# Optimization experiments

Hardware: AMD Instinct MI355X
Metric: run time of the kernel (lower is better)

Reference implementation:

```python
import jax, jax.numpy as jnp
import numpy as np

DIM = 1024
HEADS = 8
DIM_HEAD = 64
INNER = HEADS * DIM_HEAD  # 512


def setup_inputs() -> dict:
    key = jax.random.key(0)
    k1, k2, k3, k4 = jax.random.split(key, 4)
    x = jax.random.normal(k1, (4, 4096, DIM), dtype=jnp.float32)
    # torch nn.Linear weights: [out_features, in_features]
    w_qkv = jax.random.normal(k2, (INNER * 3, DIM), dtype=jnp.float32) * (DIM ** -0.5)
    w_out = jax.random.normal(k3, (DIM, INNER), dtype=jnp.float32) * (INNER ** -0.5)
    b_out = jax.random.normal(k4, (DIM,), dtype=jnp.float32) * 0.01
    return {"x": x, "w_qkv": w_qkv, "w_out": w_out, "b_out": b_out}


def reference(x, w_qkv, w_out, b_out):
    b, n, _ = x.shape
    h, dh = HEADS, DIM_HEAD
    qkv = x @ w_qkv.T  # [b, n, 3*inner]
    q, k, v = jnp.split(qkv, 3, axis=-1)
    # [b, n, inner] -> [b, h, n, dh]
    reshape = lambda t: t.reshape(b, n, h, dh).transpose(0, 2, 1, 3)
    q, k, v = reshape(q), reshape(k), reshape(v)
    k = jax.nn.softmax(k, axis=-1)
    context = jnp.einsum('bhnd,bhne->bhde', k, v)   # [b, h, dh, dh]
    out = jnp.einsum('bhnd,bhde->bhne', q, context)  # [b, h, n, dh]
    out = out.transpose(0, 2, 1, 3).reshape(b, n, h * dh)
    return out @ w_out.T + b_out
```

## Files before the change

### kernel.cpp

```cpp
#include <hip/hip_runtime.h>
#include <hip/hip_bf16.h>

using bf16 = __hip_bfloat16;
typedef __attribute__((ext_vector_type(8))) short short8;
typedef __attribute__((ext_vector_type(4))) float floatx4;

#define NB 4
#define NSEQ 4096
#define DIM 1024
#define INNER 512
#define TOK (NB * NSEQ)


__device__ inline unsigned short f2bf(float x) {
  union { bf16 h; unsigned short u; } c; c.h = __float2bfloat16(x); return c.u;
}
__device__ inline float bf2f(unsigned short u) {
  return __uint_as_float((unsigned)u << 16);
}
__device__ inline uint4 pack8(const float4 a, const float4 b) {
  union { uint4 u; unsigned short h[8]; } p;
  p.h[0] = f2bf(a.x); p.h[1] = f2bf(a.y); p.h[2] = f2bf(a.z); p.h[3] = f2bf(a.w);
  p.h[4] = f2bf(b.x); p.h[5] = f2bf(b.y); p.h[6] = f2bf(b.z); p.h[7] = f2bf(b.w);
  return p.u;
}

__device__ inline void gload_lds16(const bf16* g, bf16* ldsbase) {
  __builtin_amdgcn_global_load_lds(
      (const __attribute__((address_space(1))) void*)g,
      (__attribute__((address_space(3))) void*)ldsbase, 16, 0, 0);
}

__global__ __launch_bounds__(256)
void conv_wkv(const float* __restrict__ w_qkv, bf16* __restrict__ wkvb) {
  const size_t i = (size_t)blockIdx.x * 256 + threadIdx.x;
  const float* src = w_qkv + (size_t)INNER * DIM + i * 8;
  const float4 a = ((const float4*)src)[0];
  const float4 b = ((const float4*)src)[1];
  *(uint4*)(wkvb + i * 8) = pack8(a, b);
}

__global__ __launch_bounds__(256, 4)
void kv_softmax_ctx(const float* __restrict__ x, const bf16* __restrict__ wkvb,
                    float* __restrict__ ctx_part) {
  __shared__ __align__(16) char smem[33280];
  bf16* As = (bf16*)smem;
  bf16* Bs = (bf16*)(smem + 16384);
  unsigned short* skT = (unsigned short*)smem;
  unsigned short* vT  = (unsigned short*)(smem + 16640);

  const int tid    = threadIdx.x;
  const int p      = blockIdx.x;
  const int h      = (p >> 3) & 7;
  const int m_tile = (p & 7) + (p >> 6) * 8;
  const int m0     = m_tile * 128;

  const int wave = tid >> 6;
  const int lane = tid & 63;
  const int wr   = (wave >> 1) * 64;
  const int wc   = (wave & 1) * 64;
  const int quad = lane >> 4;
  const int r16  = lane & 15;
  const int rxor = r16 & 7;
  const int lrow = lane >> 3;
  const int lcol = lane & 7;
  const int gchunk = lcol ^ lrow;
  const int wb   = wave * 8 + lrow;

  const float* Ax = x + (size_t)(m0 + wb) * 1024 + lcol * 8;

  floatx4 acc[4][4];
#pragma unroll
  for (int i = 0; i < 4; ++i)
#pragma unroll
    for (int j = 0; j < 4; ++j) acc[i][j] = (floatx4)0.0f;

  for (int kt = 0; kt < 16; ++kt) {
    const int k0 = kt << 6;
#pragma unroll
    for (int t = 0; t < 4; ++t) {
      const int s   = wave * 4 + t;
      const int row = s * 8 + lrow;
      const int badd = (s * 8 >= 64) ? (448 + h * 64) : (h * 64);
      gload_lds16(wkvb + (size_t)(badd + row) * 1024 + k0 + gchunk * 8, Bs + s * 512);
    }
    float4 rA[8];
#pragma unroll
    for (int l = 0; l < 4; ++l) {
      rA[2 * l]     = *(const float4*)(Ax + (size_t)l * 32768 + k0);
      rA[2 * l + 1] = *(const float4*)(Ax + (size_t)l * 32768 + k0 + 4);
    }
#pragma unroll
    for (int l = 0; l < 4; ++l) {
      const int row = l * 32 + wb;
      *(uint4*)(As + row * 64 + ((lcol ^ lrow) << 3)) = pack8(rA[2 * l], rA[2 * l + 1]);
    }
    __syncthreads();
#pragma unroll
    for (int kk = 0; kk < 64; kk += 32) {
      const int cbase = kk >> 3;
      short8 af[4], bfg[4];
#pragma unroll
      for (int i = 0; i < 4; ++i)
        af[i] = *(const short8*)(As + (wr + i * 16 + r16) * 64 + (((quad + cbase) ^ rxor) << 3));
#pragma unroll
      for (int j = 0; j < 4; ++j)
        bfg[j] = *(const short8*)(Bs + (wc + j * 16 + r16) * 64 + (((quad + cbase) ^ rxor) << 3));
#pragma unroll
      for (int i = 0; i < 4; ++i)
#pragma unroll
        for (int j = 0; j < 4; ++j)
          acc[i][j] = __builtin_amdgcn_mfma_f32_16x16x32_bf16(af[i], bfg[j], acc[i][j], 0, 0, 0);
    }
    __syncthreads();
  }

  const int rowbase = wr + quad * 4;
  if ((wave & 1) == 0) {
#pragma unroll
    for (int i = 0; i < 4; ++i)
#pragma unroll
      for (int reg = 0; reg < 4; ++reg) {
        float kf[4];
#pragma unroll
        for (int j = 0; j < 4; ++j) kf[j] = bf2f(f2bf(acc[i][j][reg]));
        float mx = fmaxf(fmaxf(kf[0], kf[1]), fmaxf(kf[2], kf[3]));
        mx = fmaxf(mx, __shfl_xor(mx, 1, 64));
        mx = fmaxf(mx, __shfl_xor(mx, 2, 64));
        mx = fmaxf(mx, __shfl_xor(mx, 4, 64));
        mx = fmaxf(mx, __shfl_xor(mx, 8, 64));
        float e[4]; float s = 0.0f;
#pragma unroll
        for (int j = 0; j < 4; ++j) { e[j] = __expf(kf[j] - mx); s += e[j]; }
        s += __shfl_xor(s, 1, 64);
        s += __shfl_xor(s, 2, 64);
        s += __shfl_xor(s, 4, 64);
        s += __shfl_xor(s, 8, 64);
        const float inv = 1.0f / s;
        const int row = rowbase + i * 16 + reg;
#pragma unroll
        for (int j = 0; j < 4; ++j)
          skT[(j * 16 + r16) * 130 + row] = f2bf(e[j] * inv);
      }
  } else {
#pragma unroll
    for (int i = 0; i < 4; ++i)
#pragma unroll
      for (int reg = 0; reg < 4; ++reg) {
        const int row = rowbase + i * 16 + reg;
#pragma unroll
        for (int j = 0; j < 4; ++j)
          vT[(j * 16 + r16) * 130 + row] = f2bf(acc[i][j][reg]);
      }
  }
  __syncthreads();

  const int d0 = wave * 16;
  floatx4 cacc[4];
#pragma unroll
  for (int j = 0; j < 4; ++j) cacc[j] = (floatx4)0.0f;
#pragma unroll
  for (int kk = 0; kk < 4; ++kk) {
    const int kof = kk * 32 + quad * 8;
    union { short8 v; unsigned u[4]; } afr;
    {
      const unsigned* qa = (const unsigned*)(skT + (d0 + r16) * 130 + kof);
      afr.u[0] = qa[0]; afr.u[1] = qa[1]; afr.u[2] = qa[2]; afr.u[3] = qa[3];
    }
#pragma unroll
    for (int j = 0; j < 4; ++j) {
      union { short8 v; unsigned u[4]; } bfr;
      const unsigned* qb = (const unsigned*)(vT + (j * 16 + r16) * 130 + kof);
      bfr.u[0] = qb[0]; bfr.u[1] = qb[1]; bfr.u[2] = qb[2]; bfr.u[3] = qb[3];
      cacc[j] = __builtin_amdgcn_mfma_f32_16x16x32_bf16(afr.v, bfr.v, cacc[j], 0, 0, 0);
    }
  }

  float* cg = ctx_part + (size_t)(m_tile * 8 + h) * 4096;
#pragma unroll
  for (int j = 0; j < 4; ++j) {
    const int e = j * 16 + r16;
#pragma unroll
    for (int r = 0; r < 4; ++r) {
      const int d = d0 + quad * 4 + r;
      cg[d * 64 + e] = cacc[j][r];
    }
  }
}

__global__ __launch_bounds__(256)
void build_m2_wqt(const float* __restrict__ w_out, const float* __restrict__ ctx_part,
                  const float* __restrict__ wq, bf16* __restrict__ M2,
                  bf16* __restrict__ wqT) {
  const int tid = threadIdx.x;
  const int blk = blockIdx.x;

  if (blk < 256) {
    __shared__ unsigned short wo_s[128 * 68];
    __shared__ __align__(16) float ctx_s[4096];

    const int bh = blk >> 3;
    const int b  = bh >> 3, h = bh & 7;
    const int o0 = (blk & 7) * 128;

#pragma unroll
    for (int l = 0; l < 8; ++l) {
      const int s = l * 256 + tid;
      const int row = s >> 4, col4 = s & 15;
      const float4 v = *(const float4*)(w_out + (size_t)(o0 + row) * 512 + h * 64 + col4 * 4);
      wo_s[row * 68 + col4 * 4 + 0] = f2bf(v.x);
      wo_s[row * 68 + col4 * 4 + 1] = f2bf(v.y);
      wo_s[row * 68 + col4 * 4 + 2] = f2bf(v.z);
      wo_s[row * 68 + col4 * 4 + 3] = f2bf(v.w);
    }
    const float4* cg = (const float4*)(ctx_part + (size_t)(b * 256 + h) * 4096);
#pragma unroll
    for (int l = 0; l < 4; ++l) {
      const int idx = l * 256 + tid;
      float4 s = make_float4(0.f, 0.f, 0.f, 0.f);
#pragma unroll
      for (int sl = 0; sl < 32; ++sl) {
        const float4 v = cg[(size_t)sl * 8192 + idx];
        s.x += v.x; s.y += v.y; s.z += v.z; s.w += v.w;
      }
      ((float4*)ctx_s)[idx] = s;
    }
    __syncthreads();

    const int o_loc = tid & 127;
    const int dbase = (tid >> 7) * 32;
    float acc[32];
#pragma unroll
    for (int d = 0; d < 32; ++d) acc[d] = 0.0f;

    for (int e = 0; e < 64; ++e) {
      const float wf = bf2f(wo_s[o_loc * 68 + e]);
#pragma unroll
      for (int d = 0; d < 32; ++d)
        acc[d] += wf * ctx_s[(dbase + d) * 64 + e];
    }

    union { uint4 u[4]; unsigned short hh[32]; } o;
#pragma unroll
    for (int d = 0; d < 32; ++d) o.hh[d] = f2bf(acc[d]);
    unsigned short* dst = (unsigned short*)M2 + (size_t)(b * 1024 + o0 + o_loc) * 512 + h * 64 + dbase;
#pragma unroll
    for (int i = 0; i < 4; ++i) ((uint4*)dst)[i] = o.u[i];
  } else {
    __shared__ unsigned short t[64 * 68];
    const int q  = blk - 256;
    const int c0 = (q & 15) * 64;
    const int r0 = (q >> 4) * 64;
#pragma unroll
    for (int l = 0; l < 4; ++l) {
      const int s = l * 256 + tid;
      const int row = s >> 4, col4 = s & 15;
      const float4 v = *(const float4*)(wq + (size_t)(r0 + row) * 1024 + c0 + col4 * 4);
      t[row * 68 + col4 * 4 + 0] = f2bf(v.x);
      t[row * 68 + col4 * 4 + 1] = f2bf(v.y);
      t[row * 68 + col4 * 4 + 2] = f2bf(v.z);
      t[row * 68 + col4 * 4 + 3] = f2bf(v.w);
    }
    __syncthreads();
#pragma unroll
    for (int l = 0; l < 2; ++l) {
      const int s = l * 256 + tid;
      const int cc = s >> 3, g = s & 7;
      union { uint4 u; unsigned short hh[8]; } o;
#pragma unroll
      for (int u = 0; u < 8; ++u) o.hh[u] = t[(g * 8 + u) * 68 + cc];
      *(uint4*)((unsigned short*)wqT + (size_t)(c0 + cc) * 512 + r0 + g * 8) = o.u;
    }
  }
}

template <typename TO>
__global__ __launch_bounds__(256, 4)
void gemm_bt(const bf16* __restrict__ A, int lda,
             const bf16* __restrict__ W, int mTiles,
             TO* __restrict__ C, int ldc, int K,
             TO* __restrict__ Calt, int msplit) {
  __shared__ __align__(16) bf16 As[128 * 64];
  __shared__ __align__(16) bf16 Bs[128 * 64];

  const int tid    = threadIdx.x;
  const int p      = blockIdx.x;
  const int m_tile = p % mTiles;
  const int n_tile = p / mTiles;
  const int m0     = m_tile * 128;
  const int n0     = n_tile * 128;

  const int wave = tid >> 6;
  const int lane = tid & 63;
  const int wr   = (wave >> 1) * 64;
  const int wc   = (wave & 1) * 64;
  const int quad = lane >> 4;
  const int r16  = lane & 15;
  const int rxor = r16 & 7;
  const int lrow = lane >> 3;
  const int lcol = lane & 7;
  const int gchunk = lcol ^ lrow;

  floatx4 acc[4][4];
#pragma unroll
  for (int i = 0; i < 4; ++i)
#pragma unroll
    for (int j = 0; j < 4; ++j) acc[i][j] = (floatx4)0.0f;

  const int ksteps = K >> 6;
  for (int kt = 0; kt < ksteps; ++kt) {
    const int k0 = kt << 6;
#pragma unroll
    for (int t = 0; t < 4; ++t) {
      const int s   = wave * 4 + t;
      const int row = s * 8 + lrow;
      gload_lds16(A + (size_t)(m0 + row) * lda + k0 + gchunk * 8, As + s * 512);
      gload_lds16(W + (size_t)(n0 + row) * K   + k0 + gchunk * 8, Bs + s * 512);
    }
    __syncthreads();
#pragma unroll
    for (int kk = 0; kk < 64; kk += 32) {
      const int cbase = kk >> 3;
      short8 af[4], bfg[4];
#pragma unroll
      for (int i = 0; i < 4; ++i)
        af[i] = *(const short8*)(As + (wr + i * 16 + r16) * 64 + (((quad + cbase) ^ rxor) << 3));
#pragma unroll
      for (int j = 0; j < 4; ++j)
        bfg[j] = *(const short8*)(Bs + (wc + j * 16 + r16) * 64 + (((quad + cbase) ^ rxor) << 3));
#pragma unroll
      for (int i = 0; i < 4; ++i)
#pragma unroll
        for (int j = 0; j < 4; ++j)
          acc[i][j] = __builtin_amdgcn_mfma_f32_16x16x32_bf16(af[i], bfg[j], acc[i][j], 0, 0, 0);
    }
    __syncthreads();
  }

  TO* Cb = C; int radj = 0;
  if (Calt && m0 >= msplit) { Cb = Calt; radj = msplit; }
#pragma unroll
  for (int j = 0; j < 4; ++j) {
    const int col = n0 + wc + j * 16 + r16;
#pragma unroll
    for (int i = 0; i < 4; ++i) {
      const int rowb = m0 + wr + i * 16 + quad * 4 - radj;
#pragma unroll
      for (int r = 0; r < 4; ++r)
        Cb[(size_t)(rowb + r) * ldc + col] = __float2bfloat16(acc[i][j][r]);
    }
  }
}

__global__ __launch_bounds__(256, 4)
void gemm_f32a(const float* __restrict__ A,
               const bf16* __restrict__ W, size_t wbatch,
               const bf16* __restrict__ Walt,
               const float* __restrict__ bias,
               float* __restrict__ C, int ldc) {
  __shared__ __align__(16) bf16 As[128 * 64];
  __shared__ __align__(16) bf16 Bs[128 * 64];

  const int tid    = threadIdx.x;
  const int p      = blockIdx.x;
  const int n_tile = (p >> 3) & 7;
  const int m_tile = (p & 7) + (p >> 6) * 8;
  const int m0 = m_tile * 128, n0 = n_tile * 128;
  const int batch = m_tile >> 5;
  const bf16* Wp = (batch == 3 && Walt) ? Walt : W + (size_t)batch * wbatch;

  const int wave = tid >> 6;
  const int lane = tid & 63;
  const int wr   = (wave >> 1) * 64;
  const int wc   = (wave & 1) * 64;
  const int quad = lane >> 4;
  const int r16  = lane & 15;
  const int rxor = r16 & 7;
  const int lrow = lane >> 3;
  const int lcol = lane & 7;
  const int gchunk = lcol ^ lrow;
  const int wb = wave * 8 + lrow;

  const float* Ax = A + (size_t)(m0 + wb) * 1024 + lcol * 8;

  floatx4 acc[4][4];
#pragma unroll
  for (int i = 0; i < 4; ++i)
#pragma unroll
    for (int j = 0; j < 4; ++j) acc[i][j] = (floatx4)0.0f;

  for (int kt = 0; kt < 16; ++kt) {
    const int k0 = kt << 6;
#pragma unroll
    for (int t = 0; t < 4; ++t) {
      const int s   = wave * 4 + t;
      const int row = s * 8 + lrow;
      gload_lds16(Wp + (size_t)(n0 + row) * 1024 + k0 + gchunk * 8, Bs + s * 512);
    }
    float4 rA[8];
#pragma unroll
    for (int l = 0; l < 4; ++l) {
      rA[2 * l]     = *(const float4*)(Ax + (size_t)l * 32768 + k0);
      rA[2 * l + 1] = *(const float4*)(Ax + (size_t)l * 32768 + k0 + 4);
    }
#pragma unroll
    for (int l = 0; l < 4; ++l) {
      const int row = l * 32 + wb;
      *(uint4*)(As + row * 64 + ((lcol ^ lrow) << 3)) = pack8(rA[2 * l], rA[2 * l + 1]);
    }
    __syncthreads();
#pragma unroll
    for (int kk = 0; kk < 64; kk += 32) {
      const int cbase = kk >> 3;
      short8 af[4], bfg[4];
#pragma unroll
      for (int i = 0; i < 4; ++i)
        af[i] = *(const short8*)(As + (wr + i * 16 + r16) * 64 + (((quad + cbase) ^ rxor) << 3));
#pragma unroll
      for (int j = 0; j < 4; ++j)
        bfg[j] = *(const short8*)(Bs + (wc + j * 16 + r16) * 64 + (((quad + cbase) ^ rxor) << 3));
#pragma unroll
      for (int i = 0; i < 4; ++i)
#pragma unroll
        for (int j = 0; j < 4; ++j)
          acc[i][j] = __builtin_amdgcn_mfma_f32_16x16x32_bf16(af[i], bfg[j], acc[i][j], 0, 0, 0);
    }
    __syncthreads();
  }

#pragma unroll
  for (int j = 0; j < 4; ++j) {
    const int col = n0 + wc + j * 16 + r16;
    const float bv = bias[col];
#pragma unroll
    for (int i = 0; i < 4; ++i) {
      const int rowb = m0 + wr + i * 16 + quad * 4;
#pragma unroll
      for (int r = 0; r < 4; ++r)
        C[(size_t)(rowb + r) * ldc + col] = acc[i][j][r] + bv;
    }
  }
}

extern "C" void kernel_launch(void* const* d_in, const int* in_sizes, int n_in,
                              void* d_out, int out_size, void* d_ws, size_t ws_size,
                              hipStream_t stream) {
  const float* x     = (const float*)d_in[0];
  const float* w_qkv = (const float*)d_in[1];
  const float* w_out = (const float*)d_in[2];
  const float* b_out = (const float*)d_in[3];
  float* out = (float*)d_out;

  char* wbuf = (char*)d_in[1];
  char* obuf = (char*)d_out;

  float* ctxp = (float*)obuf;
  bf16*  M2   = (bf16*)(obuf + (size_t)16777216);
  bf16*  wqT  = (bf16*)(obuf + (size_t)20971520);
  bf16*  wkvb = (bf16*)(obuf + (size_t)23068672);
  bf16*  W2   = (bf16*)wbuf;
  bf16*  W2b3 = (bf16*)d_in[2];

  conv_wkv<<<512, 256, 0, stream>>>(w_qkv, wkvb);

  kv_softmax_ctx<<<1024, 256, 0, stream>>>(x, wkvb, ctxp);

  build_m2_wqt<<<384, 256, 0, stream>>>(w_out, ctxp, w_qkv, M2, wqT);

  gemm_bt<bf16><<<256, 256, 0, stream>>>(
      M2, 512, wqT, 32, W2, 1024, 512, W2b3, 3072);

  gemm_f32a<<<1024, 256, 0, stream>>>(
      x, W2, (size_t)1048576, W2b3, b_out, out, DIM);
}
```

Baseline: 260.0 us.

## Pre-convert x to bf16 and stream it into LDS with direct global loads

A new prep kernel converts all of x to bf16 in a workspace, converts Wkv, and transposes Wq, replacing the old conv_wkv kernel and taking the Wq transpose out of the M2 builder. The kv/softmax/context kernel then loads its A tile with global_load_lds, as it already does for B, instead of loading fp32 registers and packing them into LDS. This cuts register pressure and VALU conversion work in the main GEMM loop. The cost is an extra full pass over x: a 64MB read plus a 32MB bf16 write, while the later fp32 GEMM still reads the original x.

```diff
diff --git a/kernel.cpp b/kernel.cpp
--- a/kernel.cpp
+++ b/kernel.cpp
@@ -32,16 +32,50 @@
 }
 
 __global__ __launch_bounds__(256)
-void conv_wkv(const float* __restrict__ w_qkv, bf16* __restrict__ wkvb) {
-  const size_t i = (size_t)blockIdx.x * 256 + threadIdx.x;
-  const float* src = w_qkv + (size_t)INNER * DIM + i * 8;
-  const float4 a = ((const float4*)src)[0];
-  const float4 b = ((const float4*)src)[1];
-  *(uint4*)(wkvb + i * 8) = pack8(a, b);
+void fused_prep(const float* __restrict__ x, const float* __restrict__ w_qkv,
+                bf16* __restrict__ xb, bf16* __restrict__ wkvb,
+                bf16* __restrict__ wqT) {
+  const int tid = threadIdx.x;
+  const int blk = blockIdx.x;
+
+  if (blk < 8192) {
+    const size_t i = (size_t)blk * 256 + tid;
+    const float* src = x + i * 8;
+    *(uint4*)(xb + i * 8) = pack8(((const float4*)src)[0], ((const float4*)src)[1]);
+  } else if (blk < 8704) {
+    const size_t i = (size_t)(blk - 8192) * 256 + tid;
+    const float* src = w_qkv + (size_t)INNER * DIM + i * 8;
+    *(uint4*)(wkvb + i * 8) = pack8(((const float4*)src)[0], ((const float4*)src)[1]);
+  } else {
+    __shared__ unsigned short t[64 * 68];
+    const int q  = blk - 8704;
+    const int c0 = (q & 15) * 64;
+    const int r0 = (q >> 4) * 64;
+#pragma unroll
+    for (int l = 0; l < 4; ++l) {
+      const int s = l * 256 + tid;
+      const int row = s >> 4, col4 = s & 15;
+      const float4 v = *(const float4*)(w_qkv + (size_t)(r0 + row) * 1024 + c0 + col4 * 4);
+      t[row * 68 + col4 * 4 + 0] = f2bf(v.x);
+      t[row * 68 + col4 * 4 + 1] = f2bf(v.y);
+      t[row * 68 + col4 * 4 + 2] = f2bf(v.z);
+      t[row * 68 + col4 * 4 + 3] = f2bf(v.w);
+    }
+    __syncthreads();
+#pragma unroll
+    for (int l = 0; l < 2; ++l) {
+      const int s = l * 256 + tid;
+      const int cc = s >> 3, g = s & 7;
+      union { uint4 u; unsigned short h[8]; } o;
+#pragma unroll
+      for (int u = 0; u < 8; ++u) o.h[u] = t[(g * 8 + u) * 68 + cc];
+      *(uint4*)((unsigned short*)wqT + (size_t)(c0 + cc) * 512 + r0 + g * 8) = o.u;
+    }
+  }
 }
 
 __global__ __launch_bounds__(256, 4)
-void kv_softmax_ctx(const float* __restrict__ x, const bf16* __restrict__ wkvb,
+void kv_softmax_ctx(const bf16* __restrict__ A, const bf16* __restrict__ Wkv,
                     float* __restrict__ ctx_part) {
   __shared__ __align__(16) char smem[33280];
   bf16* As = (bf16*)smem;
@@ -65,9 +99,6 @@
   const int lrow = lane >> 3;
   const int lcol = lane & 7;
   const int gchunk = lcol ^ lrow;
-  const int wb   = wave * 8 + lrow;
-
-  const float* Ax = x + (size_t)(m0 + wb) * 1024 + lcol * 8;
 
   floatx4 acc[4][4];
 #pragma unroll
@@ -82,18 +113,8 @@
       const int s   = wave * 4 + t;
       const int row = s * 8 + lrow;
       const int badd = (s * 8 >= 64) ? (448 + h * 64) : (h * 64);
-      gload_lds16(wkvb + (size_t)(badd + row) * 1024 + k0 + gchunk * 8, Bs + s * 512);
-    }
-    float4 rA[8];
-#pragma unroll
-    for (int l = 0; l < 4; ++l) {
-      rA[2 * l]     = *(const float4*)(Ax + (size_t)l * 32768 + k0);
-      rA[2 * l + 1] = *(const float4*)(Ax + (size_t)l * 32768 + k0 + 4);
-    }
-#pragma unroll
-    for (int l = 0; l < 4; ++l) {
-      const int row = l * 32 + wb;
-      *(uint4*)(As + row * 64 + ((lcol ^ lrow) << 3)) = pack8(rA[2 * l], rA[2 * l + 1]);
+      gload_lds16(A   + (size_t)(m0 + row) * 1024 + k0 + gchunk * 8, As + s * 512);
+      gload_lds16(Wkv + (size_t)(badd + row) * 1024 + k0 + gchunk * 8, Bs + s * 512);
     }
     __syncthreads();
 #pragma unroll
@@ -189,89 +210,59 @@
 }
 
 __global__ __launch_bounds__(256)
-void build_m2_wqt(const float* __restrict__ w_out, const float* __restrict__ ctx_part,
-                  const float* __restrict__ wq, bf16* __restrict__ M2,
-                  bf16* __restrict__ wqT) {
+void build_m2(const float* __restrict__ w_out, const float* __restrict__ ctx_part,
+              bf16* __restrict__ M2) {
+  __shared__ unsigned short wo_s[128 * 68];
+  __shared__ __align__(16) float ctx_s[4096];
+
   const int tid = threadIdx.x;
-  const int blk = blockIdx.x;
-
-  if (blk < 256) {
-    __shared__ unsigned short wo_s[128 * 68];
-    __shared__ __align__(16) float ctx_s[4096];
-
-    const int bh = blk >> 3;
-    const int b  = bh >> 3, h = bh & 7;
-    const int o0 = (blk & 7) * 128;
-
-#pragma unroll
-    for (int l = 0; l < 8; ++l) {
-      const int s = l * 256 + tid;
-      const int row = s >> 4, col4 = s & 15;
-      const float4 v = *(const float4*)(w_out + (size_t)(o0 + row) * 512 + h * 64 + col4 * 4);
-      wo_s[row * 68 + col4 * 4 + 0] = f2bf(v.x);
-      wo_s[row * 68 + col4 * 4 + 1] = f2bf(v.y);
-      wo_s[row * 68 + col4 * 4 + 2] = f2bf(v.z);
-      wo_s[row * 68 + col4 * 4 + 3] = f2bf(v.w);
-    }
-    const float4* cg = (const float4*)(ctx_part + (size_t)(b * 256 + h) * 4096);
-#pragma unroll
-    for (int l = 0; l < 4; ++l) {
-      const int idx = l * 256 + tid;
-      float4 s = make_float4(0.f, 0.f, 0.f, 0.f);
-#pragma unroll
-      for (int sl = 0; sl < 32; ++sl) {
-        const float4 v = cg[(size_t)sl * 8192 + idx];
-        s.x += v.x; s.y += v.y; s.z += v.z; s.w += v.w;
-      }
-      ((float4*)ctx_s)[idx] = s;
-    }
-    __syncthreads();
-
-    const int o_loc = tid & 127;
-    const int dbase = (tid >> 7) * 32;
-    float acc[32];
-#pragma unroll
-    for (int d = 0; d < 32; ++d) acc[d] = 0.0f;
-
-    for (int e = 0; e < 64; ++e) {
-      const float wf = bf2f(wo_s[o_loc * 68 + e]);
-#pragma unroll
-      for (int d = 0; d < 32; ++d)
-        acc[d] += wf * ctx_s[(dbase + d) * 64 + e];
-    }
-
-    union { uint4 u[4]; unsigned short hh[32]; } o;
-#pragma unroll
-    for (int d = 0; d < 32; ++d) o.hh[d] = f2bf(acc[d]);
-    unsigned short* dst = (unsigned short*)M2 + (size_t)(b * 1024 + o0 + o_loc) * 512 + h * 64 + dbase;
-#pragma unroll
-    for (int i = 0; i < 4; ++i) ((uint4*)dst)[i] = o.u[i];
-  } else {
-    __shared__ unsigned short t[64 * 68];
-    const int q  = blk - 256;
-    const int c0 = (q & 15) * 64;
-    const int r0 = (q >> 4) * 64;
-#pragma unroll
-    for (int l = 0; l < 4; ++l) {
-      const int s = l * 256 + tid;
-      const int row = s >> 4, col4 = s & 15;
-      const float4 v = *(const float4*)(wq + (size_t)(r0 + row) * 1024 + c0 + col4 * 4);
-      t[row * 68 + col4 * 4 + 0] = f2bf(v.x);
-      t[row * 68 + col4 * 4 + 1] = f2bf(v.y);
-      t[row * 68 + col4 * 4 + 2] = f2bf(v.z);
-      t[row * 68 + col4 * 4 + 3] = f2bf(v.w);
-    }
-    __syncthreads();
-#pragma unroll
-    for (int l = 0; l < 2; ++l) {
-      const int s = l * 256 + tid;
-      const int cc = s >> 3, g = s & 7;
-      union { uint4 u; unsigned short hh[8]; } o;
-#pragma unroll
-      for (int u = 0; u < 8; ++u) o.hh[u] = t[(g * 8 + u) * 68 + cc];
-      *(uint4*)((unsigned short*)wqT + (size_t)(c0 + cc) * 512 + r0 + g * 8) = o.u;
-    }
-  }
+  const int bh  = blockIdx.y;
+  const int b   = bh >> 3, h = bh & 7;
+  const int o0  = blockIdx.x * 128;
+
+#pragma unroll
+  for (int l = 0; l < 8; ++l) {
+    const int s = l * 256 + tid;
+    const int row = s >> 4, col4 = s & 15;
+    const float4 v = *(const float4*)(w_out + (size_t)(o0 + row) * 512 + h * 64 + col4 * 4);
+    wo_s[row * 68 + col4 * 4 + 0] = f2bf(v.x);
+    wo_s[row * 68 + col4 * 4 + 1] = f2bf(v.y);
+    wo_s[row * 68 + col4 * 4 + 2] = f2bf(v.z);
+    wo_s[row * 68 + col4 * 4 + 3] = f2bf(v.w);
+  }
+  const float4* cg = (const float4*)(ctx_part + (size_t)(b * 256 + h) * 4096);
+#pragma unroll
+  for (int l = 0; l < 4; ++l) {
+    const int idx = l * 256 + tid;
+    float4 s = make_float4(0.f, 0.f, 0.f, 0.f);
+#pragma unroll
+    for (int sl = 0; sl < 32; ++sl) {
+      const float4 v = cg[(size_t)sl * 8192 + idx];
+      s.x += v.x; s.y += v.y; s.z += v.z; s.w += v.w;
+    }
+    ((float4*)ctx_s)[idx] = s;
+  }
+  __syncthreads();
+
+  const int o_loc = tid & 127;
+  const int dbase = (tid >> 7) * 32;
+  float acc[32];
+#pragma unroll
+  for (int d = 0; d < 32; ++d) acc[d] = 0.0f;
+
+  for (int e = 0; e < 64; ++e) {
+    const float wf = bf2f(wo_s[o_loc * 68 + e]);
+#pragma unroll
+    for (int d = 0; d < 32; ++d)
+      acc[d] += wf * ctx_s[(dbase + d) * 64 + e];
+  }
+
+  union { uint4 u[4]; unsigned short hh[32]; } o;
+#pragma unroll
+  for (int d = 0; d < 32; ++d) o.hh[d] = f2bf(acc[d]);
+  unsigned short* dst = (unsigned short*)M2 + (size_t)(b * 1024 + o0 + o_loc) * 512 + h * 64 + dbase;
+#pragma unroll
+  for (int i = 0; i < 4; ++i) ((uint4*)dst)[i] = o.u[i];
 }
 
 template <typename TO>
@@ -454,18 +445,19 @@
   char* wbuf = (char*)d_in[1];
   char* obuf = (char*)d_out;
 
-  float* ctxp = (float*)obuf;
-  bf16*  M2   = (bf16*)(obuf + (size_t)16777216);
-  bf16*  wqT  = (bf16*)(obuf + (size_t)20971520);
-  bf16*  wkvb = (bf16*)(obuf + (size_t)23068672);
+  bf16*  xb   = (bf16*)obuf;
+  float* ctxp = (float*)(obuf + (size_t)33554432);
+  bf16*  wkvb = (bf16*)(obuf + (size_t)50331648);
+  bf16*  M2   = (bf16*)(obuf + (size_t)52428800);
+  bf16*  wqT  = (bf16*)(obuf + (size_t)56623104);
   bf16*  W2   = (bf16*)wbuf;
   bf16*  W2b3 = (bf16*)d_in[2];
 
-  conv_wkv<<<512, 256, 0, stream>>>(w_qkv, wkvb);
-
-  kv_softmax_ctx<<<1024, 256, 0, stream>>>(x, wkvb, ctxp);
-
-  build_m2_wqt<<<384, 256, 0, stream>>>(w_out, ctxp, w_qkv, M2, wqT);
+  fused_prep<<<8832, 256, 0, stream>>>(x, w_qkv, xb, wkvb, wqT);
+
+  kv_softmax_ctx<<<1024, 256, 0, stream>>>(xb, wkvb, ctxp);
+
+  build_m2<<<dim3(8, 32), 256, 0, stream>>>(w_out, ctxp, M2);
 
   gemm_bt<bf16><<<256, 256, 0, stream>>>(
       M2, 512, wqT, 32, W2, 1024, 512, W2b3, 3072);
```

Result: no change. 264.3 us (+1.7%).
